# Kernel tuning notes

Hardware: AMD Instinct MI355X
Metric: run time of the kernel (lower is better)

Reference implementation:

```python
import jax, jax.numpy as jnp
import numpy as np

H = 256        # hidden_channels
G = 13         # num_input_geofeature
E = 100000     # number of 2nd-order triplets
N = 50000      # num_nodes
DEPTH = 3      # finaldepth
EPS = 1e-5     # BatchNorm eps


def setup_inputs() -> dict:
    key = jax.random.key(0)
    ks = jax.random.split(key, 10)
    d_in = 3 * H + G  # 781
    return {
        "node_feature": jax.random.normal(ks[0], (N, H), jnp.float32),
        "geo_encoding": jax.random.normal(ks[1], (E, G), jnp.float32),
        "edge_index_2rd": jax.random.randint(ks[2], (3, E), 0, N),
        "edx_ij": jax.random.randint(ks[3], (E,), 0, 2 * E),
        "edx_jk": jax.random.randint(ks[4], (E,), 0, 2 * E),
        "att": jax.random.uniform(ks[5], (4,), jnp.float32),
        # 4 branches: layer0 (d_in->H) + DEPTH layers (H->H), xavier-ish init, zero bias
        "W0": jax.random.normal(ks[6], (4, d_in, H), jnp.float32) * (1.0 / np.sqrt(d_in)),
        "b0": jnp.zeros((4, H), jnp.float32),
        "Wh": jax.random.normal(ks[7], (4, DEPTH, H, H), jnp.float32) * (1.0 / np.sqrt(H)),
        "bh": jnp.zeros((4, DEPTH, H), jnp.float32),
        # BatchNorm (eval mode): affine params + running stats, one per layer per branch
        "gamma": jnp.ones((4, DEPTH + 1, H), jnp.float32),
        "beta": jnp.zeros((4, DEPTH + 1, H), jnp.float32),
        "run_mean": jnp.zeros((4, DEPTH + 1, H), jnp.float32),
        "run_var": jnp.ones((4, DEPTH + 1, H), jnp.float32),
        "num_edge_inside": E,
        "num_nodes": N,
    }


def _bn(h, g, b, m, v):
    return (h - m) * jax.lax.rsqrt(v + EPS) * g + b


def reference(node_feature, geo_encoding, edge_index_2rd, edx_ij, edx_jk, att,
              W0, b0, Wh, bh, gamma, beta, run_mean, run_var,
              num_edge_inside, num_nodes):
    i, j, k = edge_index_2rd[0], edge_index_2rd[1], edge_index_2rd[2]
    # gather node triplets + geo features -> [E, 3H+G]
    x = jnp.concatenate(
        [node_feature[i], node_feature[j], node_feature[k], geo_encoding], axis=-1)

    m_ij = edx_ij < num_edge_inside
    m_jk = edx_jk < num_edge_inside
    # 4 mutually-exclusive, exhaustive routing masks: [4, E]
    masks = jnp.stack([m_ij & m_jk, m_ij & ~m_jk, ~m_ij & m_jk, ~m_ij & ~m_jk])

    x_output = jnp.zeros((x.shape[0], H), x.dtype)
    for br in range(4):  # fixed small branch count
        h = jax.nn.relu(_bn(x @ W0[br] + b0[br],
                            gamma[br, 0], beta[br, 0], run_mean[br, 0], run_var[br, 0]))
        for l in range(DEPTH):
            h = jax.nn.relu(_bn(h @ Wh[br, l] + bh[br, l],
                                gamma[br, l + 1], beta[br, l + 1],
                                run_mean[br, l + 1], run_var[br, l + 1]))
        h = jax.nn.leaky_relu(h) * att[br]
        x_output = x_output + jnp.where(masks[br][:, None], h, jnp.zeros((), h.dtype))
    # scatter_add over target node index i -> [num_nodes, H]
    return jax.ops.segment_sum(x_output, i, num_segments=num_nodes)
```

## Files before the change

### kernel.cpp

```cpp
#include <hip/hip_runtime.h>
#include <hip/hip_bf16.h>
#include <stdint.h>

#define HCH 256
#define GEO 13
#define DEPTH 3
#define EPSBN 1e-5f

typedef __attribute__((ext_vector_type(8))) short short8;
typedef __attribute__((ext_vector_type(4))) float floatx4;

__device__ __forceinline__ short f2bs(float f) {
    unsigned u = __float_as_uint(f);
    unsigned r = (u + 0x7fffu + ((u >> 16) & 1u)) >> 16;
    return (short)r;
}

__global__ void k_zero(float4* out4, int n4, int* cnt) {
    int i = blockIdx.x * blockDim.x + threadIdx.x;
    if (i < n4) out4[i] = make_float4(0.f, 0.f, 0.f, 0.f);
    if (blockIdx.x == 0 && threadIdx.x < 4) cnt[threadIdx.x] = 0;
}

__global__ void k_prep(const float* __restrict__ W0, const float* __restrict__ Wh,
                       const float* __restrict__ b0, const float* __restrict__ bh,
                       const float* __restrict__ gm, const float* __restrict__ bt,
                       const float* __restrict__ mn, const float* __restrict__ vr,
                       const float* __restrict__ att,
                       const float* __restrict__ node, const float* __restrict__ geo,
                       const int* __restrict__ edx_ij, const int* __restrict__ edx_jk,
                       const int* __restrict__ nei_p,
                       short* __restrict__ W0t, short* __restrict__ Wht,
                       float* __restrict__ sc, float* __restrict__ of,
                       short* __restrict__ node_bf, short* __restrict__ geo_bf,
                       int* __restrict__ lists, int* __restrict__ cnt,
                       int E, int d_in_dim, int nb_node, int nb_geo) {
    const int B_W0 = 100, B_WH = 96, B_SC = 16;
    __shared__ short s[32][256];
    int b = blockIdx.x, t = threadIdx.x;
    if (b < B_W0) {
        int c = b % 25, br = b / 25;
        #pragma unroll
        for (int kk = 0; kk < 32; ++kk) {
            int kidx = c * 32 + kk;
            float v = (kidx < d_in_dim) ? W0[((size_t)br * d_in_dim + kidx) * HCH + t] : 0.f;
            s[kk][t] = f2bs(v);
        }
        __syncthreads();
        size_t obase = ((size_t)(b) * 256 + t) * 32;
        #pragma unroll
        for (int g = 0; g < 4; ++g) {
            short8 v;
            #pragma unroll
            for (int j = 0; j < 8; ++j) v[j] = s[g * 8 + j][t];
            *reinterpret_cast<short8*>(W0t + obase + g * 8) = v;
        }
    } else if (b < B_W0 + B_WH) {
        int idx = b - B_W0;
        int c = idx & 7; idx >>= 3;
        int l = idx % 3, br = idx / 3;
        #pragma unroll
        for (int kk = 0; kk < 32; ++kk) {
            float v = Wh[((size_t)(br * DEPTH + l) * HCH + (c * 32 + kk)) * HCH + t];
            s[kk][t] = f2bs(v);
        }
        __syncthreads();
        size_t obase = ((size_t)(b - B_W0) * 256 + t) * 32;
        #pragma unroll
        for (int g = 0; g < 4; ++g) {
            short8 v;
            #pragma unroll
            for (int j = 0; j < 8; ++j) v[j] = s[g * 8 + j][t];
            *reinterpret_cast<short8*>(Wht + obase + g * 8) = v;
        }
    } else if (b < B_W0 + B_WH + B_SC) {
        int idx = (b - B_W0 - B_WH) * 256 + t;
        int col = idx & 255, l = (idx >> 8) & 3, br = idx >> 10;
        int gi = (br * (DEPTH + 1) + l) * HCH + col;
        float sA = gm[gi] * rsqrtf(vr[gi] + EPSBN);
        float bias = (l == 0) ? b0[br * HCH + col] : bh[(br * DEPTH + (l - 1)) * HCH + col];
        float ofv = (bias - mn[gi]) * sA + bt[gi];
        if (l == 3) { float av = att[br]; sA *= av; ofv *= av; }
        sc[idx] = sA;
        of[idx] = ofv;
    } else if (b < B_W0 + B_WH + B_SC + nb_node) {
        size_t i = ((size_t)(b - B_W0 - B_WH - B_SC) * 256 + t) * 8;
        const float4* src = reinterpret_cast<const float4*>(node + i);
        float4 v0 = src[0], v1 = src[1];
        short8 pk;
        pk[0] = f2bs(v0.x); pk[1] = f2bs(v0.y); pk[2] = f2bs(v0.z); pk[3] = f2bs(v0.w);
        pk[4] = f2bs(v1.x); pk[5] = f2bs(v1.y); pk[6] = f2bs(v1.z); pk[7] = f2bs(v1.w);
        *reinterpret_cast<short8*>(node_bf + i) = pk;
    } else if (b < B_W0 + B_WH + B_SC + nb_node + nb_geo) {
        int i = (b - B_W0 - B_WH - B_SC - nb_node) * 256 + t;
        int e = i >> 2, cc = i & 3;
        if (e < E) {
            short8 pk;
            #pragma unroll
            for (int j = 0; j < 8; ++j) {
                int col = cc * 8 + j;
                pk[j] = (col < GEO) ? f2bs(geo[(size_t)e * GEO + col]) : (short)0;
            }
            *reinterpret_cast<short8*>(geo_bf + (size_t)e * 32 + cc * 8) = pk;
        }
    } else {
        int e = (b - (B_W0 + B_WH + B_SC + nb_node + nb_geo)) * 256 + t;
        int NEI = nei_p[0];
        int lane = t & 63;
        int br = -1;
        if (e < E)
            br = ((edx_ij[e] < NEI) ? 0 : 2) + ((edx_jk[e] < NEI) ? 0 : 1);
        unsigned long long lt = (lane == 63) ? 0x7fffffffffffffffull
                                             : ((1ull << lane) - 1ull);
        #pragma unroll
        for (int bb = 0; bb < 4; ++bb) {
            unsigned long long mk = __ballot(br == bb);
            if (mk) {
                int leader = __ffsll((long long)mk) - 1;
                int base = 0;
                if (lane == leader) base = atomicAdd(&cnt[bb], (int)__popcll(mk));
                base = __shfl(base, leader);
                if (br == bb) {
                    int pos = base + (int)__popcll(mk & lt);
                    lists[(size_t)bb * E + pos] = e;
                }
            }
        }
    }
}

__global__ __launch_bounds__(512)
void k_main(const short* __restrict__ node_bf, const short* __restrict__ geo_bf,
            const int* __restrict__ eidx,
            const short* __restrict__ W0t, const short* __restrict__ Wht,
            const float* __restrict__ sc, const float* __restrict__ of,
            const int* __restrict__ lists, const int* __restrict__ cnt,
            float* __restrict__ out, int E) {
    __shared__ __align__(16) short A[64][264];
    __shared__ int s_i[64];
    __shared__ int s_jk[2][64];
    __shared__ int s_e[64];

    int c0 = cnt[0], c1 = cnt[1], c2 = cnt[2], c3 = cnt[3];
    int t0 = (c0 + 63) >> 6, t1 = (c1 + 63) >> 6, t2 = (c2 + 63) >> 6, t3 = (c3 + 63) >> 6;
    int b = blockIdx.x;
    int br, tile, count;
    if (b < t0)                     { br = 0; tile = b;                count = c0; }
    else if (b < t0 + t1)           { br = 1; tile = b - t0;           count = c1; }
    else if (b < t0 + t1 + t2)      { br = 2; tile = b - t0 - t1;      count = c2; }
    else if (b < t0 + t1 + t2 + t3) { br = 3; tile = b - t0 - t1 - t2; count = c3; }
    else return;
    int m = count - tile * 64; if (m > 64) m = 64;

    int t = threadIdx.x;
    if (t < 64) {
        int e = (t < m) ? lists[(size_t)br * E + (size_t)tile * 64 + t] : 0;
        s_e[t] = (t < m) ? e : -1;
        s_i[t] = eidx[e];
        s_jk[0][t] = eidx[E + e];
        s_jk[1][t] = eidx[2 * E + e];
    }
    __syncthreads();

    int wv = t >> 6, lane = t & 63, quad = lane >> 4, l16 = lane & 15;

    floatx4 acc[4][2];
    #pragma unroll
    for (int rt = 0; rt < 4; ++rt)
        #pragma unroll
        for (int ct = 0; ct < 2; ++ct)
            #pragma unroll
            for (int r = 0; r < 4; ++r) acc[rt][ct][r] = 0.f;

    int boff[2];
    #pragma unroll
    for (int ct = 0; ct < 2; ++ct)
        boff[ct] = (wv * 32 + ct * 16 + l16) * 32 + quad * 8;

    auto do_chunks = [&](const short* Wbase, int nch) {
        short8 bcur[2], bnxt[2];
        #pragma unroll
        for (int ct = 0; ct < 2; ++ct)
            bcur[ct] = *reinterpret_cast<const short8*>(Wbase + boff[ct]);
        for (int c = 0; c < nch; ++c) {
            if (c + 1 < nch) {
                const short* Bn = Wbase + (size_t)(c + 1) * 8192;
                #pragma unroll
                for (int ct = 0; ct < 2; ++ct)
                    bnxt[ct] = *reinterpret_cast<const short8*>(Bn + boff[ct]);
            }
            short8 af[4];
            #pragma unroll
            for (int rt = 0; rt < 4; ++rt)
                af[rt] = *reinterpret_cast<const short8*>(&A[rt * 16 + l16][c * 32 + quad * 8]);
            #pragma unroll
            for (int rt = 0; rt < 4; ++rt)
                #pragma unroll
                for (int ct = 0; ct < 2; ++ct)
                    acc[rt][ct] = __builtin_amdgcn_mfma_f32_16x16x32_bf16(
                        af[rt], bcur[ct], acc[rt][ct], 0, 0, 0);
            if (c + 1 < nch) {
                #pragma unroll
                for (int ct = 0; ct < 2; ++ct) bcur[ct] = bnxt[ct];
            }
        }
    };

    for (int p = 0; p < 4; ++p) {
        __syncthreads();
        if (p < 3) {
            const int* idxs = (p == 0) ? s_i : s_jk[p - 1];
            #pragma unroll
            for (int it = 0; it < 4; ++it) {
                int job = it * 512 + t;
                int row = job >> 5, cc = job & 31;
                short8 v = *reinterpret_cast<const short8*>(
                    node_bf + (size_t)idxs[row] * HCH + cc * 8);
                *reinterpret_cast<short8*>(&A[row][cc * 8]) = v;
            }
        } else {
            if (t < 256) {
                int row = t >> 2, cc = t & 3;
                int e = s_e[row];
                short8 v;
                if (e >= 0)
                    v = *reinterpret_cast<const short8*>(geo_bf + (size_t)e * 32 + cc * 8);
                else
                    #pragma unroll
                    for (int j = 0; j < 8; ++j) v[j] = 0;
                *reinterpret_cast<short8*>(&A[row][cc * 8]) = v;
            }
        }
        __syncthreads();
        do_chunks(W0t + (size_t)(br * 25 + ((p < 3) ? p * 8 : 24)) * 8192, (p < 3) ? 8 : 1);
    }

    for (int l = 0; l < 4; ++l) {
        float sv[2], ov[2];
        #pragma unroll
        for (int ct = 0; ct < 2; ++ct) {
            int col = wv * 32 + ct * 16 + l16;
            sv[ct] = sc[(br * 4 + l) * HCH + col];
            ov[ct] = of[(br * 4 + l) * HCH + col];
        }
        if (l < 3) {
            __syncthreads();
            #pragma unroll
            for (int rt = 0; rt < 4; ++rt)
                #pragma unroll
                for (int ct = 0; ct < 2; ++ct) {
                    int col = wv * 32 + ct * 16 + l16;
                    #pragma unroll
                    for (int r = 0; r < 4; ++r) {
                        float h = fmaxf(acc[rt][ct][r] * sv[ct] + ov[ct], 0.f);
                        A[rt * 16 + quad * 4 + r][col] = f2bs(h);
                        acc[rt][ct][r] = 0.f;
                    }
                }
            __syncthreads();
            do_chunks(Wht + (size_t)((br * 3 + l) * 8) * 8192, 8);
        } else {
            #pragma unroll
            for (int rt = 0; rt < 4; ++rt)
                #pragma unroll
                for (int r = 0; r < 4; ++r) {
                    int row = rt * 16 + quad * 4 + r;
                    if (row < m) {
                        float* orow = out + (size_t)s_i[row] * HCH + wv * 32 + l16;
                        #pragma unroll
                        for (int ct = 0; ct < 2; ++ct) {
                            float h = fmaxf(acc[rt][ct][r] * sv[ct] + ov[ct], 0.f);
                            atomicAdd(orow + ct * 16, h);
                        }
                    }
                }
        }
    }
}

extern "C" void kernel_launch(void* const* d_in, const int* in_sizes, int n_in,
                              void* d_out, int out_size, void* d_ws, size_t ws_size,
                              hipStream_t stream) {
    const float* node  = (const float*)d_in[0];
    const float* geo   = (const float*)d_in[1];
    const int*   eidx  = (const int*)d_in[2];
    const int*   edxij = (const int*)d_in[3];
    const int*   edxjk = (const int*)d_in[4];
    const float* att   = (const float*)d_in[5];
    const float* W0    = (const float*)d_in[6];
    const float* b0    = (const float*)d_in[7];
    const float* Wh    = (const float*)d_in[8];
    const float* bh    = (const float*)d_in[9];
    const float* gm    = (const float*)d_in[10];
    const float* bt    = (const float*)d_in[11];
    const float* mn    = (const float*)d_in[12];
    const float* vr    = (const float*)d_in[13];
    const int*   neip  = (const int*)d_in[14];

    int E = in_sizes[3];
    int N = in_sizes[0] / HCH;
    int d_in_dim = in_sizes[6] / (4 * HCH);

    uint8_t* w = (uint8_t*)d_ws;
    size_t off = 0;
    short* W0t  = (short*)(w + off); off += (size_t)4 * 25 * 256 * 32 * 2;
    short* Wht  = (short*)(w + off); off += (size_t)4 * 3 * 8 * 256 * 32 * 2;
    float* sc   = (float*)(w + off); off += 4096 * 4;
    float* of   = (float*)(w + off); off += 4096 * 4;
    int*   lists= (int*)(w + off);   off += (size_t)4 * E * 4;
    int*   cnt  = (int*)(w + off);   off += 16;
    short* node_bf = (short*)(w + off); off += (size_t)N * HCH * 2;
    short* geo_bf  = (short*)(w + off); off += (size_t)E * 32 * 2;

    float* out = (float*)d_out;
    int n4 = out_size / 4;
    k_zero<<<(n4 + 255) / 256, 256, 0, stream>>>((float4*)out, n4, cnt);

    int nb_node = N / 8;
    int nb_geo  = (4 * E + 255) / 256;
    int nb_cmp  = (E + 255) / 256;
    k_prep<<<100 + 96 + 16 + nb_node + nb_geo + nb_cmp, 256, 0, stream>>>(
        W0, Wh, b0, bh, gm, bt, mn, vr, att, node, geo, edxij, edxjk, neip,
        W0t, Wht, sc, of, node_bf, geo_bf, lists, cnt, E, d_in_dim, nb_node, nb_geo);

    int T = (E >> 6) + 8;
    k_main<<<T, 512, 0, stream>>>(node_bf, geo_bf, eidx, W0t, Wht,
                                  sc, of, lists, cnt, out, E);
}
```

Before: 384.8 us.

## Double-buffer LDS staging and retile warps to 2x4 row/column grid

Adds a second LDS activation buffer so the next gather (node j/k rows, geo features) is staged while the current chunk's MFMAs run, removing one barrier per stage. Between MLP layers it writes outputs into the alternate buffer, so it drops the barrier before the write. The 8 waves are regrouped from 1x8 (each covering all 64 rows and 32 columns) into 2x4 (32 rows by 64 columns each). This halves LDS A-fragment reads per wave but doubles the B-fragment global loads per wave. LDS use doubles to about 67KB, which may cut occupancy.

Result: slower. 432.1 us (+12.3%).

```diff
diff --git a/kernel.cpp b/kernel.cpp
--- a/kernel.cpp
+++ b/kernel.cpp
@@ -136,7 +136,7 @@
             const float* __restrict__ sc, const float* __restrict__ of,
             const int* __restrict__ lists, const int* __restrict__ cnt,
             float* __restrict__ out, int E) {
-    __shared__ __align__(16) short A[64][264];
+    __shared__ __align__(16) short A[2][64][264];
     __shared__ int s_i[64];
     __shared__ int s_jk[2][64];
     __shared__ int s_e[64];
@@ -163,112 +163,120 @@
     __syncthreads();
 
     int wv = t >> 6, lane = t & 63, quad = lane >> 4, l16 = lane & 15;
-
-    floatx4 acc[4][2];
+    int rg = wv >> 2, cg = wv & 3;
+    int rowb = rg * 32;
+
+    floatx4 acc[2][4];
     #pragma unroll
-    for (int rt = 0; rt < 4; ++rt)
-        #pragma unroll
-        for (int ct = 0; ct < 2; ++ct)
+    for (int rt = 0; rt < 2; ++rt)
+        #pragma unroll
+        for (int ct = 0; ct < 4; ++ct)
             #pragma unroll
             for (int r = 0; r < 4; ++r) acc[rt][ct][r] = 0.f;
 
-    int boff[2];
+    int boff[4];
     #pragma unroll
-    for (int ct = 0; ct < 2; ++ct)
-        boff[ct] = (wv * 32 + ct * 16 + l16) * 32 + quad * 8;
-
-    auto do_chunks = [&](const short* Wbase, int nch) {
-        short8 bcur[2], bnxt[2];
-        #pragma unroll
-        for (int ct = 0; ct < 2; ++ct)
+    for (int ct = 0; ct < 4; ++ct)
+        boff[ct] = (cg * 64 + ct * 16 + l16) * 32 + quad * 8;
+
+    auto stage_node = [&](const int* idxs, short (*buf)[264]) {
+        #pragma unroll
+        for (int it = 0; it < 4; ++it) {
+            int job = it * 512 + t;
+            int row = job >> 5, cc = job & 31;
+            short8 v = *reinterpret_cast<const short8*>(
+                node_bf + (size_t)idxs[row] * HCH + cc * 8);
+            *reinterpret_cast<short8*>(&buf[row][cc * 8]) = v;
+        }
+    };
+    auto stage_geo = [&](short (*buf)[264]) {
+        if (t < 256) {
+            int row = t >> 2, cc = t & 3;
+            int e = s_e[row];
+            short8 v;
+            if (e >= 0)
+                v = *reinterpret_cast<const short8*>(geo_bf + (size_t)e * 32 + cc * 8);
+            else {
+                #pragma unroll
+                for (int j = 0; j < 8; ++j) v[j] = 0;
+            }
+            *reinterpret_cast<short8*>(&buf[row][cc * 8]) = v;
+        }
+    };
+    auto do_chunks = [&](const short* Wbase, int nch, const short (*buf)[264]) {
+        short8 bcur[4], bnxt[4];
+        #pragma unroll
+        for (int ct = 0; ct < 4; ++ct)
             bcur[ct] = *reinterpret_cast<const short8*>(Wbase + boff[ct]);
         for (int c = 0; c < nch; ++c) {
             if (c + 1 < nch) {
                 const short* Bn = Wbase + (size_t)(c + 1) * 8192;
                 #pragma unroll
-                for (int ct = 0; ct < 2; ++ct)
+                for (int ct = 0; ct < 4; ++ct)
                     bnxt[ct] = *reinterpret_cast<const short8*>(Bn + boff[ct]);
             }
-            short8 af[4];
-            #pragma unroll
-            for (int rt = 0; rt < 4; ++rt)
-                af[rt] = *reinterpret_cast<const short8*>(&A[rt * 16 + l16][c * 32 + quad * 8]);
-            #pragma unroll
-            for (int rt = 0; rt < 4; ++rt)
-                #pragma unroll
-                for (int ct = 0; ct < 2; ++ct)
+            short8 af[2];
+            #pragma unroll
+            for (int rt = 0; rt < 2; ++rt)
+                af[rt] = *reinterpret_cast<const short8*>(
+                    &buf[rowb + rt * 16 + l16][c * 32 + quad * 8]);
+            #pragma unroll
+            for (int rt = 0; rt < 2; ++rt)
+                #pragma unroll
+                for (int ct = 0; ct < 4; ++ct)
                     acc[rt][ct] = __builtin_amdgcn_mfma_f32_16x16x32_bf16(
                         af[rt], bcur[ct], acc[rt][ct], 0, 0, 0);
             if (c + 1 < nch) {
                 #pragma unroll
-                for (int ct = 0; ct < 2; ++ct) bcur[ct] = bnxt[ct];
+                for (int ct = 0; ct < 4; ++ct) bcur[ct] = bnxt[ct];
             }
         }
     };
 
+    stage_node(s_i, A[0]);
     for (int p = 0; p < 4; ++p) {
         __syncthreads();
-        if (p < 3) {
-            const int* idxs = (p == 0) ? s_i : s_jk[p - 1];
-            #pragma unroll
-            for (int it = 0; it < 4; ++it) {
-                int job = it * 512 + t;
-                int row = job >> 5, cc = job & 31;
-                short8 v = *reinterpret_cast<const short8*>(
-                    node_bf + (size_t)idxs[row] * HCH + cc * 8);
-                *reinterpret_cast<short8*>(&A[row][cc * 8]) = v;
-            }
-        } else {
-            if (t < 256) {
-                int row = t >> 2, cc = t & 3;
-                int e = s_e[row];
-                short8 v;
-                if (e >= 0)
-                    v = *reinterpret_cast<const short8*>(geo_bf + (size_t)e * 32 + cc * 8);
-                else
-                    #pragma unroll
-                    for (int j = 0; j < 8; ++j) v[j] = 0;
-                *reinterpret_cast<short8*>(&A[row][cc * 8]) = v;
-            }
-        }
-        __syncthreads();
-        do_chunks(W0t + (size_t)(br * 25 + ((p < 3) ? p * 8 : 24)) * 8192, (p < 3) ? 8 : 1);
+        if (p == 0)      stage_node(s_jk[0], A[1]);
+        else if (p == 1) stage_node(s_jk[1], A[0]);
+        else if (p == 2) stage_geo(A[1]);
+        do_chunks(W0t + (size_t)(br * 25 + ((p < 3) ? p * 8 : 24)) * 8192,
+                  (p < 3) ? 8 : 1, A[p & 1]);
     }
 
     for (int l = 0; l < 4; ++l) {
-        float sv[2], ov[2];
-        #pragma unroll
-        for (int ct = 0; ct < 2; ++ct) {
-            int col = wv * 32 + ct * 16 + l16;
+        float sv[4], ov[4];
+        #pragma unroll
+        for (int ct = 0; ct < 4; ++ct) {
+            int col = cg * 64 + ct * 16 + l16;
             sv[ct] = sc[(br * 4 + l) * HCH + col];
             ov[ct] = of[(br * 4 + l) * HCH + col];
         }
         if (l < 3) {
-            __syncthreads();
-            #pragma unroll
-            for (int rt = 0; rt < 4; ++rt)
-                #pragma unroll
-                for (int ct = 0; ct < 2; ++ct) {
-                    int col = wv * 32 + ct * 16 + l16;
+            short (*dst)[264] = A[l & 1];
+            #pragma unroll
+            for (int rt = 0; rt < 2; ++rt)
+                #pragma unroll
+                for (int ct = 0; ct < 4; ++ct) {
+                    int col = cg * 64 + ct * 16 + l16;
                     #pragma unroll
                     for (int r = 0; r < 4; ++r) {
                         float h = fmaxf(acc[rt][ct][r] * sv[ct] + ov[ct], 0.f);
-                        A[rt * 16 + quad * 4 + r][col] = f2bs(h);
+                        dst[rowb + rt * 16 + quad * 4 + r][col] = f2bs(h);
                         acc[rt][ct][r] = 0.f;
                     }
                 }
             __syncthreads();
-            do_chunks(Wht + (size_t)((br * 3 + l) * 8) * 8192, 8);
+            do_chunks(Wht + (size_t)((br * 3 + l) * 8) * 8192, 8, dst);
         } else {
             #pragma unroll
-            for (int rt = 0; rt < 4; ++rt)
+            for (int rt = 0; rt < 2; ++rt)
                 #pragma unroll
                 for (int r = 0; r < 4; ++r) {
-                    int row = rt * 16 + quad * 4 + r;
+                    int row = rowb + rt * 16 + quad * 4 + r;
                     if (row < m) {
-                        float* orow = out + (size_t)s_i[row] * HCH + wv * 32 + l16;
+                        float* orow = out + (size_t)s_i[row] * HCH + cg * 64 + l16;
                         #pragma unroll
-                        for (int ct = 0; ct < 2; ++ct) {
+                        for (int ct = 0; ct < 4; ++ct) {
                             float h = fmaxf(acc[rt][ct][r] * sv[ct] + ov[ct], 0.f);
                             atomicAdd(orow + ct * 16, h);
                         }
```

## Restructure MLP kernel to per-wave 32-edge tiles with register-resident activations

Applied to the files above, without the earlier changes.

Each wave now processes 32 edges independently, with weights as the MFMA A operand and gathered features as B. Activations stay in registers between layers and are passed through cross-lane shuffles instead of LDS with block barriers. The BatchNorm scale and the att factor are folded into the bf16 weights, and the layer-0 bias enters through an extra constant-one geo column. This removes shared-memory staging and __syncthreads, but every wave streams the full weight set from cache and uses many more accumulator registers.

Result: slower. 721.6 us (+87.5%).

```diff
diff --git a/kernel.cpp b/kernel.cpp
--- a/kernel.cpp
+++ b/kernel.cpp
@@ -1,19 +1,25 @@
 #include <hip/hip_runtime.h>
-#include <hip/hip_bf16.h>
 #include <stdint.h>
 
 #define HCH 256
 #define GEO 13
 #define DEPTH 3
 #define EPSBN 1e-5f
+#define MFMA __builtin_amdgcn_mfma_f32_16x16x32_bf16
 
 typedef __attribute__((ext_vector_type(8))) short short8;
 typedef __attribute__((ext_vector_type(4))) float floatx4;
+typedef __attribute__((ext_vector_type(4))) int int4v;
 
 __device__ __forceinline__ short f2bs(float f) {
     unsigned u = __float_as_uint(f);
     unsigned r = (u + 0x7fffu + ((u >> 16) & 1u)) >> 16;
     return (short)r;
+}
+__device__ __forceinline__ unsigned pk2(float a, float b) {
+    unsigned ua = __float_as_uint(a); ua = (ua + 0x7fffu + ((ua >> 16) & 1u)) >> 16;
+    unsigned ub = __float_as_uint(b); ub = (ub + 0x7fffu + ((ub >> 16) & 1u)) & 0xffff0000u;
+    return (ua & 0xffffu) | ub;
 }
 
 __global__ void k_zero(float4* out4, int n4, int* cnt) {
@@ -40,14 +46,18 @@
     int b = blockIdx.x, t = threadIdx.x;
     if (b < B_W0) {
         int c = b % 25, br = b / 25;
+        int gi = (br * (DEPTH + 1)) * HCH + t;
+        float s0 = gm[gi] * rsqrtf(vr[gi] + EPSBN);
+        float of0 = (b0[br * HCH + t] - mn[gi]) * s0 + bt[gi];
         #pragma unroll
         for (int kk = 0; kk < 32; ++kk) {
             int kidx = c * 32 + kk;
-            float v = (kidx < d_in_dim) ? W0[((size_t)br * d_in_dim + kidx) * HCH + t] : 0.f;
+            float v = (kidx < d_in_dim) ? W0[((size_t)br * d_in_dim + kidx) * HCH + t] * s0
+                    : ((kidx == d_in_dim) ? of0 : 0.f);
             s[kk][t] = f2bs(v);
         }
         __syncthreads();
-        size_t obase = ((size_t)(b) * 256 + t) * 32;
+        size_t obase = ((size_t)b * 256 + t) * 32;
         #pragma unroll
         for (int g = 0; g < 4; ++g) {
             short8 v;
@@ -58,10 +68,13 @@
     } else if (b < B_W0 + B_WH) {
         int idx = b - B_W0;
         int c = idx & 7; idx >>= 3;
-        int l = idx % 3, br = idx / 3;
+        int lh = idx % 3, br = idx / 3;
+        int gi = (br * (DEPTH + 1) + lh + 1) * HCH + t;
+        float sl = gm[gi] * rsqrtf(vr[gi] + EPSBN);
+        if (lh == 2) sl *= att[br];
         #pragma unroll
         for (int kk = 0; kk < 32; ++kk) {
-            float v = Wh[((size_t)(br * DEPTH + l) * HCH + (c * 32 + kk)) * HCH + t];
+            float v = Wh[((size_t)(br * DEPTH + lh) * HCH + (c * 32 + kk)) * HCH + t] * sl;
             s[kk][t] = f2bs(v);
         }
         __syncthreads();
@@ -80,7 +93,7 @@
         float sA = gm[gi] * rsqrtf(vr[gi] + EPSBN);
         float bias = (l == 0) ? b0[br * HCH + col] : bh[(br * DEPTH + (l - 1)) * HCH + col];
         float ofv = (bias - mn[gi]) * sA + bt[gi];
-        if (l == 3) { float av = att[br]; sA *= av; ofv *= av; }
+        if (l == 3) ofv *= att[br];
         sc[idx] = sA;
         of[idx] = ofv;
     } else if (b < B_W0 + B_WH + B_SC + nb_node) {
@@ -99,7 +112,8 @@
             #pragma unroll
             for (int j = 0; j < 8; ++j) {
                 int col = cc * 8 + j;
-                pk[j] = (col < GEO) ? f2bs(geo[(size_t)e * GEO + col]) : (short)0;
+                pk[j] = (col < GEO) ? f2bs(geo[(size_t)e * GEO + col])
+                      : ((col == GEO) ? (short)0x3F80 : (short)0);
             }
             *reinterpret_cast<short8*>(geo_bf + (size_t)e * 32 + cc * 8) = pk;
         }
@@ -129,151 +143,137 @@
     }
 }
 
-__global__ __launch_bounds__(512)
+__global__ __launch_bounds__(256, 2)
 void k_main(const short* __restrict__ node_bf, const short* __restrict__ geo_bf,
             const int* __restrict__ eidx,
             const short* __restrict__ W0t, const short* __restrict__ Wht,
-            const float* __restrict__ sc, const float* __restrict__ of,
+            const float* __restrict__ of,
             const int* __restrict__ lists, const int* __restrict__ cnt,
             float* __restrict__ out, int E) {
-    __shared__ __align__(16) short A[64][264];
-    __shared__ int s_i[64];
-    __shared__ int s_jk[2][64];
-    __shared__ int s_e[64];
-
+    int t = threadIdx.x;
+    int wid = blockIdx.x * 4 + (t >> 6);
     int c0 = cnt[0], c1 = cnt[1], c2 = cnt[2], c3 = cnt[3];
-    int t0 = (c0 + 63) >> 6, t1 = (c1 + 63) >> 6, t2 = (c2 + 63) >> 6, t3 = (c3 + 63) >> 6;
-    int b = blockIdx.x;
-    int br, tile, count;
-    if (b < t0)                     { br = 0; tile = b;                count = c0; }
-    else if (b < t0 + t1)           { br = 1; tile = b - t0;           count = c1; }
-    else if (b < t0 + t1 + t2)      { br = 2; tile = b - t0 - t1;      count = c2; }
-    else if (b < t0 + t1 + t2 + t3) { br = 3; tile = b - t0 - t1 - t2; count = c3; }
+    int n0 = (c0 + 31) >> 5, n1 = (c1 + 31) >> 5, n2 = (c2 + 31) >> 5, n3 = (c3 + 31) >> 5;
+    int br, tile, cb;
+    if (wid < n0)                     { br = 0; tile = wid;                cb = c0; }
+    else if (wid < n0 + n1)           { br = 1; tile = wid - n0;           cb = c1; }
+    else if (wid < n0 + n1 + n2)      { br = 2; tile = wid - n0 - n1;      cb = c2; }
+    else if (wid < n0 + n1 + n2 + n3) { br = 3; tile = wid - n0 - n1 - n2; cb = c3; }
     else return;
-    int m = count - tile * 64; if (m > 64) m = 64;
-
-    int t = threadIdx.x;
-    if (t < 64) {
-        int e = (t < m) ? lists[(size_t)br * E + (size_t)tile * 64 + t] : 0;
-        s_e[t] = (t < m) ? e : -1;
-        s_i[t] = eidx[e];
-        s_jk[0][t] = eidx[E + e];
-        s_jk[1][t] = eidx[2 * E + e];
+    int m = cb - tile * 32; if (m > 32) m = 32;
+    int lane = t & 63, quad = lane >> 4, l16 = lane & 15;
+
+    const int* lb = lists + (size_t)br * E + tile * 32;
+    int e0 = lb[(l16 < m) ? l16 : 0];
+    int e1 = lb[(16 + l16 < m) ? (16 + l16) : 0];
+    bool v0 = (l16 < m), v1 = (16 + l16 < m);
+    size_t i0 = (size_t)eidx[e0],       i1 = (size_t)eidx[e1];
+    size_t j0 = (size_t)eidx[E + e0],   j1 = (size_t)eidx[E + e1];
+    size_t k0 = (size_t)eidx[2*E + e0], k1 = (size_t)eidx[2*E + e1];
+
+    floatx4 acc[2][16];
+    const floatx4 zf = {0.f, 0.f, 0.f, 0.f};
+
+    auto gemm_chunk = [&](const short* Wc0, short8 bf0, short8 bf1, bool first) {
+        const short* Wc = Wc0 + l16 * 32 + quad * 8;
+        #pragma unroll
+        for (int cb4 = 0; cb4 < 4; ++cb4) {
+            short8 a[4];
+            #pragma unroll
+            for (int u = 0; u < 4; ++u)
+                a[u] = *reinterpret_cast<const short8*>(Wc + (cb4 * 4 + u) * 512);
+            #pragma unroll
+            for (int u = 0; u < 4; ++u) {
+                int ix = cb4 * 4 + u;
+                if (first) {
+                    acc[0][ix] = MFMA(a[u], bf0, zf, 0, 0, 0);
+                    acc[1][ix] = MFMA(a[u], bf1, zf, 0, 0, 0);
+                } else {
+                    acc[0][ix] = MFMA(a[u], bf0, acc[0][ix], 0, 0, 0);
+                    acc[1][ix] = MFMA(a[u], bf1, acc[1][ix], 0, 0, 0);
+                }
+            }
+        }
+    };
+
+    const short* W0b = W0t + (size_t)br * 25 * 8192;
+    auto l0addr = [&](int c, int g) -> const short* {
+        if (c < 8)  return node_bf + (g ? i1 : i0) * HCH + c * 32 + quad * 8;
+        if (c < 16) return node_bf + (g ? j1 : j0) * HCH + (c - 8) * 32 + quad * 8;
+        if (c < 24) return node_bf + (g ? k1 : k0) * HCH + (c - 16) * 32 + quad * 8;
+        return geo_bf + (size_t)(g ? e1 : e0) * 32 + quad * 8;
+    };
+    short8 bg[3][2];
+    bg[0][0] = *reinterpret_cast<const short8*>(l0addr(0, 0));
+    bg[0][1] = *reinterpret_cast<const short8*>(l0addr(0, 1));
+    bg[1][0] = *reinterpret_cast<const short8*>(l0addr(1, 0));
+    bg[1][1] = *reinterpret_cast<const short8*>(l0addr(1, 1));
+    #pragma unroll
+    for (int c = 0; c < 25; ++c) {
+        if (c + 2 < 25) {
+            bg[(c + 2) % 3][0] = *reinterpret_cast<const short8*>(l0addr(c + 2, 0));
+            bg[(c + 2) % 3][1] = *reinterpret_cast<const short8*>(l0addr(c + 2, 1));
+        }
+        gemm_chunk(W0b + (size_t)c * 8192, bg[c % 3][0], bg[c % 3][1], c == 0);
     }
-    __syncthreads();
-
-    int wv = t >> 6, lane = t & 63, quad = lane >> 4, l16 = lane & 15;
-
-    floatx4 acc[4][2];
+
+    int sA = ((quad & 1) * 2) * 16 + l16;
+    int sB = sA + 16;
+    bool hi = (quad >> 1) != 0;
+
     #pragma unroll
-    for (int rt = 0; rt < 4; ++rt)
-        #pragma unroll
-        for (int ct = 0; ct < 2; ++ct)
-            #pragma unroll
-            for (int r = 0; r < 4; ++r) acc[rt][ct][r] = 0.f;
-
-    int boff[2];
+    for (int lh = 0; lh < 3; ++lh) {
+        unsigned ph[2][16][2];
+        #pragma unroll
+        for (int ct = 0; ct < 16; ++ct) {
+            float4 o = make_float4(0.f, 0.f, 0.f, 0.f);
+            if (lh > 0)
+                o = *reinterpret_cast<const float4*>(
+                        of + (br * 4 + lh) * HCH + ct * 16 + quad * 4);
+            #pragma unroll
+            for (int g = 0; g < 2; ++g) {
+                float h0 = fmaxf(acc[g][ct][0] + o.x, 0.f);
+                float h1 = fmaxf(acc[g][ct][1] + o.y, 0.f);
+                float h2 = fmaxf(acc[g][ct][2] + o.z, 0.f);
+                float h3 = fmaxf(acc[g][ct][3] + o.w, 0.f);
+                ph[g][ct][0] = pk2(h0, h1);
+                ph[g][ct][1] = pk2(h2, h3);
+            }
+        }
+        int4v bB[2][8];
+        #pragma unroll
+        for (int g = 0; g < 2; ++g)
+            #pragma unroll
+            for (int c = 0; c < 8; ++c)
+                #pragma unroll
+                for (int jp = 0; jp < 4; ++jp) {
+                    int src = (jp < 2) ? sA : sB;
+                    int tA = __shfl((int)ph[g][2 * c][jp & 1], src);
+                    int tB = __shfl((int)ph[g][2 * c + 1][jp & 1], src);
+                    bB[g][c][jp] = hi ? tB : tA;
+                }
+        const short* Wl = Wht + (size_t)((br * 3 + lh) * 8) * 8192;
+        #pragma unroll
+        for (int c = 0; c < 8; ++c)
+            gemm_chunk(Wl + (size_t)c * 8192,
+                       __builtin_bit_cast(short8, bB[0][c]),
+                       __builtin_bit_cast(short8, bB[1][c]), c == 0);
+    }
+
+    float* o0 = out + i0 * HCH;
+    float* o1 = out + i1 * HCH;
     #pragma unroll
-    for (int ct = 0; ct < 2; ++ct)
-        boff[ct] = (wv * 32 + ct * 16 + l16) * 32 + quad * 8;
-
-    auto do_chunks = [&](const short* Wbase, int nch) {
-        short8 bcur[2], bnxt[2];
-        #pragma unroll
-        for (int ct = 0; ct < 2; ++ct)
-            bcur[ct] = *reinterpret_cast<const short8*>(Wbase + boff[ct]);
-        for (int c = 0; c < nch; ++c) {
-            if (c + 1 < nch) {
-                const short* Bn = Wbase + (size_t)(c + 1) * 8192;
-                #pragma unroll
-                for (int ct = 0; ct < 2; ++ct)
-                    bnxt[ct] = *reinterpret_cast<const short8*>(Bn + boff[ct]);
-            }
-            short8 af[4];
-            #pragma unroll
-            for (int rt = 0; rt < 4; ++rt)
-                af[rt] = *reinterpret_cast<const short8*>(&A[rt * 16 + l16][c * 32 + quad * 8]);
-            #pragma unroll
-            for (int rt = 0; rt < 4; ++rt)
-                #pragma unroll
-                for (int ct = 0; ct < 2; ++ct)
-                    acc[rt][ct] = __builtin_amdgcn_mfma_f32_16x16x32_bf16(
-                        af[rt], bcur[ct], acc[rt][ct], 0, 0, 0);
-            if (c + 1 < nch) {
-                #pragma unroll
-                for (int ct = 0; ct < 2; ++ct) bcur[ct] = bnxt[ct];
-            }
-        }
-    };
-
-    for (int p = 0; p < 4; ++p) {
-        __syncthreads();
-        if (p < 3) {
-            const int* idxs = (p == 0) ? s_i : s_jk[p - 1];
-            #pragma unroll
-            for (int it = 0; it < 4; ++it) {
-                int job = it * 512 + t;
-                int row = job >> 5, cc = job & 31;
-                short8 v = *reinterpret_cast<const short8*>(
-                    node_bf + (size_t)idxs[row] * HCH + cc * 8);
-                *reinterpret_cast<short8*>(&A[row][cc * 8]) = v;
-            }
-        } else {
-            if (t < 256) {
-                int row = t >> 2, cc = t & 3;
-                int e = s_e[row];
-                short8 v;
-                if (e >= 0)
-                    v = *reinterpret_cast<const short8*>(geo_bf + (size_t)e * 32 + cc * 8);
-                else
-                    #pragma unroll
-                    for (int j = 0; j < 8; ++j) v[j] = 0;
-                *reinterpret_cast<short8*>(&A[row][cc * 8]) = v;
-            }
-        }
-        __syncthreads();
-        do_chunks(W0t + (size_t)(br * 25 + ((p < 3) ? p * 8 : 24)) * 8192, (p < 3) ? 8 : 1);
-    }
-
-    for (int l = 0; l < 4; ++l) {
-        float sv[2], ov[2];
-        #pragma unroll
-        for (int ct = 0; ct < 2; ++ct) {
-            int col = wv * 32 + ct * 16 + l16;
-            sv[ct] = sc[(br * 4 + l) * HCH + col];
-            ov[ct] = of[(br * 4 + l) * HCH + col];
-        }
-        if (l < 3) {
-            __syncthreads();
-            #pragma unroll
-            for (int rt = 0; rt < 4; ++rt)
-                #pragma unroll
-                for (int ct = 0; ct < 2; ++ct) {
-                    int col = wv * 32 + ct * 16 + l16;
-                    #pragma unroll
-                    for (int r = 0; r < 4; ++r) {
-                        float h = fmaxf(acc[rt][ct][r] * sv[ct] + ov[ct], 0.f);
-                        A[rt * 16 + quad * 4 + r][col] = f2bs(h);
-                        acc[rt][ct][r] = 0.f;
-                    }
-                }
-            __syncthreads();
-            do_chunks(Wht + (size_t)((br * 3 + l) * 8) * 8192, 8);
-        } else {
-            #pragma unroll
-            for (int rt = 0; rt < 4; ++rt)
-                #pragma unroll
-                for (int r = 0; r < 4; ++r) {
-                    int row = rt * 16 + quad * 4 + r;
-                    if (row < m) {
-                        float* orow = out + (size_t)s_i[row] * HCH + wv * 32 + l16;
-                        #pragma unroll
-                        for (int ct = 0; ct < 2; ++ct) {
-                            float h = fmaxf(acc[rt][ct][r] * sv[ct] + ov[ct], 0.f);
-                            atomicAdd(orow + ct * 16, h);
-                        }
-                    }
-                }
+    for (int ct = 0; ct < 16; ++ct) {
+        float4 o = *reinterpret_cast<const float4*>(
+                       of + (br * 4 + 3) * HCH + ct * 16 + quad * 4);
+        #pragma unroll
+        for (int r = 0; r < 4; ++r) {
+            float ov = (r == 0) ? o.x : (r == 1) ? o.y : (r == 2) ? o.z : o.w;
+            float h0 = fmaxf(acc[0][ct][r] + ov, 0.f);
+            float h1 = fmaxf(acc[1][ct][r] + ov, 0.f);
+            int col = ct * 16 + quad * 4 + r;
+            if (v0) atomicAdd(o0 + col, h0);
+            if (v1) atomicAdd(o1 + col, h1);
         }
     }
 }
@@ -323,7 +323,8 @@
         W0, Wh, b0, bh, gm, bt, mn, vr, att, node, geo, edxij, edxjk, neip,
         W0t, Wht, sc, of, node_bf, geo_bf, lists, cnt, E, d_in_dim, nb_node, nb_geo);
 
-    int T = (E >> 6) + 8;
-    k_main<<<T, 512, 0, stream>>>(node_bf, geo_bf, eidx, W0t, Wht,
-                                  sc, of, lists, cnt, out, E);
-}
+    int maxT = (E + 31) / 32 + 4;
+    int blocks = (maxT + 3) / 4;
+    k_main<<<blocks, 256, 0, stream>>>(node_bf, geo_bf, eidx, W0t, Wht,
+                                       of, lists, cnt, out, E);
+}
```

## Prefetch next gathered node rows into registers during MFMA and deepen weight prefetch

Applied to the files above, without the earlier changes.

Gathers of the next node-feature slice (j, k, then geo) are issued into registers before the current chunk's MFMA loop, so global gather latency overlaps with compute instead of stalling between phases. The weight B-fragment prefetch becomes a fully unrolled, three-deep register ring (two chunks ahead), and the single-chunk geo case gets its own specialised path. This adds register pressure from the extra short8 buffers, which may reduce occupancy.

New measurement: 384.5 us. No clear change (-0.1%).

```diff
diff --git a/kernel.cpp b/kernel.cpp
--- a/kernel.cpp
+++ b/kernel.cpp
@@ -6,6 +6,7 @@
 #define GEO 13
 #define DEPTH 3
 #define EPSBN 1e-5f
+#define MFMA __builtin_amdgcn_mfma_f32_16x16x32_bf16
 
 typedef __attribute__((ext_vector_type(8))) short short8;
 typedef __attribute__((ext_vector_type(4))) float floatx4;
@@ -163,6 +164,7 @@
     __syncthreads();
 
     int wv = t >> 6, lane = t & 63, quad = lane >> 4, l16 = lane & 15;
+    int rbase = t >> 5, cc8 = (t & 31) * 8;
 
     floatx4 acc[4][2];
     #pragma unroll
@@ -177,17 +179,20 @@
     for (int ct = 0; ct < 2; ++ct)
         boff[ct] = (wv * 32 + ct * 16 + l16) * 32 + quad * 8;
 
-    auto do_chunks = [&](const short* Wbase, int nch) {
-        short8 bcur[2], bnxt[2];
-        #pragma unroll
-        for (int ct = 0; ct < 2; ++ct)
-            bcur[ct] = *reinterpret_cast<const short8*>(Wbase + boff[ct]);
-        for (int c = 0; c < nch; ++c) {
-            if (c + 1 < nch) {
-                const short* Bn = Wbase + (size_t)(c + 1) * 8192;
+    auto do_chunks8 = [&](const short* Wbase) {
+        short8 bb[3][2];
+        #pragma unroll
+        for (int ct = 0; ct < 2; ++ct) {
+            bb[0][ct] = *reinterpret_cast<const short8*>(Wbase + boff[ct]);
+            bb[1][ct] = *reinterpret_cast<const short8*>(Wbase + 8192 + boff[ct]);
+        }
+        #pragma unroll
+        for (int c = 0; c < 8; ++c) {
+            if (c + 2 < 8) {
+                const short* Bn = Wbase + (size_t)(c + 2) * 8192;
                 #pragma unroll
                 for (int ct = 0; ct < 2; ++ct)
-                    bnxt[ct] = *reinterpret_cast<const short8*>(Bn + boff[ct]);
+                    bb[(c + 2) % 3][ct] = *reinterpret_cast<const short8*>(Bn + boff[ct]);
             }
             short8 af[4];
             #pragma unroll
@@ -197,42 +202,61 @@
             for (int rt = 0; rt < 4; ++rt)
                 #pragma unroll
                 for (int ct = 0; ct < 2; ++ct)
-                    acc[rt][ct] = __builtin_amdgcn_mfma_f32_16x16x32_bf16(
-                        af[rt], bcur[ct], acc[rt][ct], 0, 0, 0);
-            if (c + 1 < nch) {
-                #pragma unroll
-                for (int ct = 0; ct < 2; ++ct) bcur[ct] = bnxt[ct];
-            }
+                    acc[rt][ct] = MFMA(af[rt], bb[c % 3][ct], acc[rt][ct], 0, 0, 0);
         }
     };
-
+    auto do_chunk1 = [&](const short* Wbase) {
+        short8 bc[2];
+        #pragma unroll
+        for (int ct = 0; ct < 2; ++ct)
+            bc[ct] = *reinterpret_cast<const short8*>(Wbase + boff[ct]);
+        short8 af[4];
+        #pragma unroll
+        for (int rt = 0; rt < 4; ++rt)
+            af[rt] = *reinterpret_cast<const short8*>(&A[rt * 16 + l16][quad * 8]);
+        #pragma unroll
+        for (int rt = 0; rt < 4; ++rt)
+            #pragma unroll
+            for (int ct = 0; ct < 2; ++ct)
+                acc[rt][ct] = MFMA(af[rt], bc[ct], acc[rt][ct], 0, 0, 0);
+    };
+
+    short8 g[2][4];
+    short8 ggeo;
+    {
+        #pragma unroll
+        for (int it = 0; it < 4; ++it)
+            g[0][it] = *reinterpret_cast<const short8*>(
+                node_bf + (size_t)s_i[it * 16 + rbase] * HCH + cc8);
+    }
+    int grow = t >> 2, gcc = t & 3;
     for (int p = 0; p < 4; ++p) {
         __syncthreads();
         if (p < 3) {
-            const int* idxs = (p == 0) ? s_i : s_jk[p - 1];
-            #pragma unroll
-            for (int it = 0; it < 4; ++it) {
-                int job = it * 512 + t;
-                int row = job >> 5, cc = job & 31;
-                short8 v = *reinterpret_cast<const short8*>(
-                    node_bf + (size_t)idxs[row] * HCH + cc * 8);
-                *reinterpret_cast<short8*>(&A[row][cc * 8]) = v;
+            #pragma unroll
+            for (int it = 0; it < 4; ++it)
+                *reinterpret_cast<short8*>(&A[it * 16 + rbase][cc8]) = g[p & 1][it];
+        } else if (t < 256) {
+            *reinterpret_cast<short8*>(&A[grow][gcc * 8]) = ggeo;
+        }
+        __syncthreads();
+        if (p < 2) {
+            const int* idxs = s_jk[p];
+            #pragma unroll
+            for (int it = 0; it < 4; ++it)
+                g[(p + 1) & 1][it] = *reinterpret_cast<const short8*>(
+                    node_bf + (size_t)idxs[it * 16 + rbase] * HCH + cc8);
+        } else if (p == 2 && t < 256) {
+            int e = s_e[grow];
+            if (e >= 0)
+                ggeo = *reinterpret_cast<const short8*>(geo_bf + (size_t)e * 32 + gcc * 8);
+            else {
+                #pragma unroll
+                for (int j = 0; j < 8; ++j) ggeo[j] = 0;
             }
-        } else {
-            if (t < 256) {
-                int row = t >> 2, cc = t & 3;
-                int e = s_e[row];
-                short8 v;
-                if (e >= 0)
-                    v = *reinterpret_cast<const short8*>(geo_bf + (size_t)e * 32 + cc * 8);
-                else
-                    #pragma unroll
-                    for (int j = 0; j < 8; ++j) v[j] = 0;
-                *reinterpret_cast<short8*>(&A[row][cc * 8]) = v;
-            }
-        }
-        __syncthreads();
-        do_chunks(W0t + (size_t)(br * 25 + ((p < 3) ? p * 8 : 24)) * 8192, (p < 3) ? 8 : 1);
+        }
+        if (p < 3) do_chunks8(W0t + (size_t)(br * 25 + p * 8) * 8192);
+        else       do_chunk1(W0t + (size_t)(br * 25 + 24) * 8192);
     }
 
     for (int l = 0; l < 4; ++l) {
@@ -258,7 +282,7 @@
                     }
                 }
             __syncthreads();
-            do_chunks(Wht + (size_t)((br * 3 + l) * 8) * 8192, 8);
+            do_chunks8(Wht + (size_t)((br * 3 + l) * 8) * 8192);
         } else {
             #pragma unroll
             for (int rt = 0; rt < 4; ++rt)
```
